# Kernel optimization log

Measured on AMD Instinct MI355X. Metric: run time of the kernel, lower is better.

The kernel has to match this reference:

```python
import jax, jax.numpy as jnp
import numpy as np

B, N, F_IN, F_OUT = 8, 2048, 256, 64
ALPHA = 0.2          # LeakyReLU negative slope
NEG_INF = -9e15      # matches -9000000000000000.0 in the torch code


def setup_inputs() -> dict:
    key = jax.random.key(0)
    k = jax.random.split(key, 7)
    x = jax.random.normal(k[0], (B, N, F_IN), dtype=jnp.float32)
    adj = jax.random.randint(k[1], (B, N, N), 0, 2, dtype=jnp.int32)
    # W: nn.Linear(in_features, out_features)
    W = jax.random.normal(k[2], (F_IN, F_OUT), dtype=jnp.float32) / np.sqrt(F_IN)
    b_W = jax.random.normal(k[3], (F_OUT,), dtype=jnp.float32) * 0.01
    # a: nn.Linear(2*out_features, 1); decomposed as a_src (first F_OUT rows,
    # multiplies h_i) and a_dst (last F_OUT rows, multiplies h_j) + bias.
    a_src = jax.random.normal(k[4], (F_OUT,), dtype=jnp.float32) / np.sqrt(2 * F_OUT)
    a_dst = jax.random.normal(k[5], (F_OUT,), dtype=jnp.float32) / np.sqrt(2 * F_OUT)
    a_b = jax.random.normal(k[6], (), dtype=jnp.float32) * 0.01
    return {"x": x, "adj": adj, "W": W, "b_W": b_W,
            "a_src": a_src, "a_dst": a_dst, "a_b": a_b}


def reference(x, adj, W, b_W, a_src, a_dst, a_b):
    # h = W(input): [B, N, F_OUT]
    h = jnp.einsum('bnf,fo->bno', x, W) + b_W
    # Additive attention decomposition: a([h_i || h_j]) = a_src.h_i + a_dst.h_j + b
    # (avoids materializing the [B, N, N, 2F] concat tensor of the original)
    src = jnp.einsum('bno,o->bn', h, a_src)  # row term  (h_i)
    dst = jnp.einsum('bno,o->bn', h, a_dst)  # col term  (h_j)
    e = jax.nn.leaky_relu(src[:, :, None] + dst[:, None, :] + a_b, ALPHA)  # [B,N,N]
    e = jnp.where(adj > 0, e, NEG_INF)
    attention = jax.nn.softmax(e, axis=2)
    h_prime = jnp.einsum('bij,bjo->bio', attention, h)  # [B, N, F_OUT]
    return jax.nn.elu(h_prime)  # concat=True branch
```

## Files before the change

### kernel.cpp

```cpp
#include <hip/hip_runtime.h>

#define B_   8
#define N_   2048
#define FIN  256
#define FOUT 64
#define ALPHA 0.2f

typedef __attribute__((ext_vector_type(8))) short bf16x8;
typedef __attribute__((ext_vector_type(8))) unsigned short u16x8;
typedef __attribute__((ext_vector_type(4))) unsigned short u16x4;
typedef __attribute__((ext_vector_type(4))) float f32x4;

__device__ __forceinline__ float b2f(unsigned short u) {
    union { unsigned int u; float f; } v; v.u = ((unsigned int)u) << 16; return v.f;
}
__device__ __forceinline__ unsigned short f2b(float f) {
    union { float f; unsigned int u; } v; v.f = f;
    unsigned int r = v.u + 0x7FFFu + ((v.u >> 16) & 1u);
    return (unsigned short)(r >> 16);
}

__global__ __launch_bounds__(256) void k_hgemm_tr(
    const float* __restrict__ x, const float* __restrict__ W,
    const float* __restrict__ bW, const float* __restrict__ asrc,
    const float* __restrict__ adst,
    unsigned short* __restrict__ hT, float* __restrict__ src, float* __restrict__ dst)
{
    __shared__ unsigned short tileT[FOUT * 20];
    __shared__ float as_s[FOUT], ad_s[FOUT];

    const int tid = threadIdx.x;
    const int wv = tid >> 6, lane = tid & 63;
    const int quad = lane >> 4, col = lane & 15;
    const int f = wv * 16 + col;

    if (tid < FOUT) { as_s[tid] = asrc[tid]; ad_s[tid] = adst[tid]; }

    bf16x8 Bf[8];
    #pragma unroll
    for (int kk = 0; kk < 8; ++kk) {
        bf16x8 t;
        #pragma unroll
        for (int j = 0; j < 8; ++j)
            t[j] = (short)f2b(W[(kk * 32 + quad * 8 + j) * FOUT + f]);
        Bf[kk] = t;
    }
    const float bias = bW[f];
    const int r0 = blockIdx.x * 16;
    const int b = r0 >> 11;
    const int j0b = r0 & (N_ - 1);

    f32x4 acc = {0.f, 0.f, 0.f, 0.f};
    #pragma unroll
    for (int kk = 0; kk < 8; ++kk) {
        const float* xp = x + (size_t)(r0 + col) * FIN + kk * 32 + quad * 8;
        float4 x0 = *(const float4*)xp;
        float4 x1 = *(const float4*)(xp + 4);
        bf16x8 Af;
        Af[0] = (short)f2b(x0.x); Af[1] = (short)f2b(x0.y);
        Af[2] = (short)f2b(x0.z); Af[3] = (short)f2b(x0.w);
        Af[4] = (short)f2b(x1.x); Af[5] = (short)f2b(x1.y);
        Af[6] = (short)f2b(x1.z); Af[7] = (short)f2b(x1.w);
        acc = __builtin_amdgcn_mfma_f32_16x16x32_bf16(Af, Bf[kk], acc, 0, 0, 0);
    }
    #pragma unroll
    for (int reg = 0; reg < 4; ++reg)
        tileT[f * 20 + quad * 4 + reg] = f2b(acc[reg] + bias);
    __syncthreads();

    {
        const int i = tid >> 4, fb = (tid & 15) * 4;
        float sp = 0.f, dp = 0.f;
        #pragma unroll
        for (int k = 0; k < 4; ++k) {
            float hv = b2f(tileT[(fb + k) * 20 + i]);
            sp += hv * as_s[fb + k]; dp += hv * ad_s[fb + k];
        }
        sp += __shfl_xor(sp, 1); sp += __shfl_xor(sp, 2);
        sp += __shfl_xor(sp, 4); sp += __shfl_xor(sp, 8);
        dp += __shfl_xor(dp, 1); dp += __shfl_xor(dp, 2);
        dp += __shfl_xor(dp, 4); dp += __shfl_xor(dp, 8);
        if ((tid & 15) == 0) { src[r0 + i] = sp; dst[r0 + i] = dp; }
    }
    {
        const int fq = tid >> 2, ic = (tid & 3) * 4;
        unsigned short* op = hT + (size_t)(b * FOUT + fq) * N_ + j0b + ic;
        *(u16x4*)op = *(const u16x4*)&tileT[fq * 20 + ic];
    }
}

#define ATT_TILE(Aa,Ab,Ac,Ad, An0,An1,An2,An3, BfC, BfN, BUF, JT)                      \
{                                                                                      \
                   \
    const float4 Dv0 = *(const float4*)(dstbase + (JT) * 128);                         \
    const float4 Dv1 = *(const float4*)(dstbase + (JT) * 128 + 4);                     \
    const float4 Dv2 = *(const float4*)(dstbase + (JT) * 128 + 8);                     \
    const float4 Dv3 = *(const float4*)(dstbase + (JT) * 128 + 12);                    \
    const int av[16] = {Aa.x,Aa.y,Aa.z,Aa.w, Ab.x,Ab.y,Ab.z,Ab.w,                      \
                        Ac.x,Ac.y,Ac.z,Ac.w, Ad.x,Ad.y,Ad.z,Ad.w};                     \
    const float dv[16] = {Dv0.x,Dv0.y,Dv0.z,Dv0.w, Dv1.x,Dv1.y,Dv1.z,Dv1.w,            \
                          Dv2.x,Dv2.y,Dv2.z,Dv2.w, Dv3.x,Dv3.y,Dv3.z,Dv3.w};           \
    u16x8 p0, p1; float ls = 0.f;                                                      \
    _Pragma("unroll")                                                                  \
    for (int k = 0; k < 16; ++k) {                                                     \
        float e = srci + dv[k];                                                        \
        e = e > 0.f ? e : ALPHA * e;                                                   \
        float wval = av[k] > 0 ? __expf(e) : 0.f;                                      \
        unsigned short wb = f2b(wval);                                                 \
        ls += b2f(wb);         \
        if (k < 8) p0[k] = wb; else p1[k - 8] = wb;                                    \
    }                                                                                  \
    lsum += ls;                                                                        \
    {   unsigned short* q = &w_s[BUF][il * 136 + jg * 16];                             \
        *(u16x8*)q = p0; *(u16x8*)(q + 8) = p1; }                                      \
    {                          \
        const int jn = (((JT) + 1) & 3) * 128;                                         \
        An0 = *(const int4*)(adjbase + jn);                                            \
        An1 = *(const int4*)(adjbase + jn + 4);                                        \
        An2 = *(const int4*)(adjbase + jn + 8);                                        \
        An3 = *(const int4*)(adjbase + jn + 12); }                                     \
                                   \
    asm volatile("s_waitcnt lgkmcnt(0)\n\ts_barrier" ::: "memory");                    \
    {                                        \
        const int jn = (((JT) + 1) & 3) * 128;                                         \
        BfN[0] = *(const bf16x8*)(hfbase + jn);                                        \
        BfN[1] = *(const bf16x8*)(hfbase + jn + 32);                                   \
        BfN[2] = *(const bf16x8*)(hfbase + jn + 64);                                   \
        BfN[3] = *(const bf16x8*)(hfbase + jn + 96); }                                 \
    _Pragma("unroll")                                                                  \
    for (int kk = 0; kk < 4; ++kk) {                                                   \
        bf16x8 A0 = *(const bf16x8*)&w_s[BUF][col * 136 + kk * 32 + quad * 8];         \
        bf16x8 A1 = *(const bf16x8*)&w_s[BUF][(16 + col) * 136 + kk * 32 + quad * 8];  \
        acc0 = __builtin_amdgcn_mfma_f32_16x16x32_bf16(A0, BfC[kk], acc0, 0, 0, 0);    \
        acc1 = __builtin_amdgcn_mfma_f32_16x16x32_bf16(A1, BfC[kk], acc1, 0, 0, 0);    \
    }                                                                                  \
}

__global__ __launch_bounds__(256, 4) void k_attn(
    const int* __restrict__ adj, const float* __restrict__ src,
    const float* __restrict__ dst, const unsigned short* __restrict__ hT,
    const float* __restrict__ abp,
    float* __restrict__ pnum, float* __restrict__ pden)
{
    __shared__ unsigned short w_s[2][32 * 136];
    __shared__ float src_s[32];

    const int tid = threadIdx.x;
    const int wv = tid >> 6, lane = tid & 63;
    const int quad = lane >> 4, col = lane & 15;
    const int s4 = blockIdx.x & 3;
    const int g  = blockIdx.x >> 2;
    const int b  = g >> 6;
    const int i0 = (g & 63) * 32;
    const int j0 = s4 * 512;

    if (tid < 32) src_s[tid] = src[b * N_ + i0 + tid];
    __syncthreads();

    const int il = tid >> 3, jg = tid & 7;
    const float srci = src_s[il] + abp[0];
    const int* adjbase = adj + (size_t)(b * N_ + i0 + il) * N_ + j0 + jg * 16;
    const float* dstbase = dst + b * N_ + j0 + jg * 16;
    const unsigned short* hfbase = hT + (size_t)(b * FOUT + wv * 16 + col) * N_ + j0 + quad * 8;

    int4 aE0 = *(const int4*)(adjbase);
    int4 aE1 = *(const int4*)(adjbase + 4);
    int4 aE2 = *(const int4*)(adjbase + 8);
    int4 aE3 = *(const int4*)(adjbase + 12);
    int4 aO0, aO1, aO2, aO3;
    bf16x8 bfE[4], bfO[4];
    bfE[0] = *(const bf16x8*)(hfbase);
    bfE[1] = *(const bf16x8*)(hfbase + 32);
    bfE[2] = *(const bf16x8*)(hfbase + 64);
    bfE[3] = *(const bf16x8*)(hfbase + 96);

    float lsum = 0.f;
    f32x4 acc0 = {0, 0, 0, 0}, acc1 = {0, 0, 0, 0};

    ATT_TILE(aE0, aE1, aE2, aE3, aO0, aO1, aO2, aO3, bfE, bfO, 0, 0)
    ATT_TILE(aO0, aO1, aO2, aO3, aE0, aE1, aE2, aE3, bfO, bfE, 1, 1)
    ATT_TILE(aE0, aE1, aE2, aE3, aO0, aO1, aO2, aO3, bfE, bfO, 0, 2)
    ATT_TILE(aO0, aO1, aO2, aO3, aE0, aE1, aE2, aE3, bfO, bfE, 1, 3)

    lsum += __shfl_xor(lsum, 1);
    lsum += __shfl_xor(lsum, 2);
    lsum += __shfl_xor(lsum, 4);
    if (jg == 0) pden[(size_t)blockIdx.x * 32 + il] = lsum;

    float* pb = pnum + (size_t)blockIdx.x * 2048 + wv * 16 + col;
    #pragma unroll
    for (int m = 0; m < 2; ++m) {
        f32x4 a = m ? acc1 : acc0;
        #pragma unroll
        for (int reg = 0; reg < 4; ++reg)
            pb[(m * 16 + quad * 4 + reg) * 64] = a[reg];
    }
}

__global__ __launch_bounds__(256) void k_reduce(
    const float* __restrict__ pnum, const float* __restrict__ pden,
    float* __restrict__ out)
{
    const int g = blockIdx.x;
    const int tid = threadIdx.x;
    const int f = tid & 63, ro = tid >> 6;
    const size_t base = (size_t)g * 4 * 2048;
    #pragma unroll
    for (int rr = 0; rr < 8; ++rr) {
        const int row = ro * 8 + rr;
        float num = 0.f, den = 0.f;
        #pragma unroll
        for (int s = 0; s < 4; ++s) {
            num += pnum[base + (size_t)s * 2048 + row * 64 + f];
            den += pden[(size_t)(g * 4 + s) * 32 + row];
        }
        den = den > 0.f ? den : 1.f;
        float v = num / den;
        v = v > 0.f ? v : (__expf(v) - 1.f);
        out[((size_t)g * 32 + row) * 64 + f] = v;
    }
}

extern "C" void kernel_launch(void* const* d_in, const int* in_sizes, int n_in,
                              void* d_out, int out_size, void* d_ws, size_t ws_size,
                              hipStream_t stream)
{
    const float* x    = (const float*)d_in[0];
    const int*   adj  = (const int*)d_in[1];
    const float* W    = (const float*)d_in[2];
    const float* bW   = (const float*)d_in[3];
    const float* asrc = (const float*)d_in[4];
    const float* adst = (const float*)d_in[5];
    const float* abp  = (const float*)d_in[6];
    float* out = (float*)d_out;

    char* ws = (char*)d_ws;
    unsigned short* hT = (unsigned short*)ws;
    float* src  = (float*)(ws + (size_t)2 * 1024 * 1024);
    float* dst  = (float*)(ws + (size_t)2 * 1024 * 1024 + 64 * 1024);
    float* pnum = (float*)(ws + (size_t)4 * 1024 * 1024);
    float* pden = (float*)(ws + (size_t)21 * 1024 * 1024);

    k_hgemm_tr<<<1024, 256, 0, stream>>>(x, W, bW, asrc, adst, hT, src, dst);
    k_attn<<<2048, 256, 0, stream>>>(adj, src, dst, hT, abp, pnum, pden);
    k_reduce<<<512, 256, 0, stream>>>(pnum, pden, out);
}
```

Before: 243.9 us.

## Compute attention weights directly in MFMA A-operand registers, removing LDS staging

The attention kernel now lays out adjacency loads so each lane computes exactly the bf16 weights it feeds as the MFMA A operand, which removes the shared-memory weight tile and the per-tile barriers. Each wave owns 16 rows and all 64 output features (four accumulators), with the block count halved and a register double-buffered loop over 32-column chunks. The reduce kernel is rewritten to use float4 loads over the new row-major partial layout. The cost is more hT loads per wave, since every wave reloads all 64 feature rows, plus higher register pressure and narrower 32-byte adjacency loads per lane.

```diff
diff --git a/kernel.cpp b/kernel.cpp
--- a/kernel.cpp
+++ b/kernel.cpp
@@ -5,6 +5,8 @@
 #define FIN  256
 #define FOUT 64
 #define ALPHA 0.2f
+#define NSP  4
+#define JC   (N_ / NSP / 32)
 
 typedef __attribute__((ext_vector_type(8))) short bf16x8;
 typedef __attribute__((ext_vector_type(8))) unsigned short u16x8;
@@ -89,111 +91,85 @@
     }
 }
 
-#define ATT_TILE(Aa,Ab,Ac,Ad, An0,An1,An2,An3, BfC, BfN, BUF, JT)                      \
-{                                                                                      \
-                   \
-    const float4 Dv0 = *(const float4*)(dstbase + (JT) * 128);                         \
-    const float4 Dv1 = *(const float4*)(dstbase + (JT) * 128 + 4);                     \
-    const float4 Dv2 = *(const float4*)(dstbase + (JT) * 128 + 8);                     \
-    const float4 Dv3 = *(const float4*)(dstbase + (JT) * 128 + 12);                    \
-    const int av[16] = {Aa.x,Aa.y,Aa.z,Aa.w, Ab.x,Ab.y,Ab.z,Ab.w,                      \
-                        Ac.x,Ac.y,Ac.z,Ac.w, Ad.x,Ad.y,Ad.z,Ad.w};                     \
-    const float dv[16] = {Dv0.x,Dv0.y,Dv0.z,Dv0.w, Dv1.x,Dv1.y,Dv1.z,Dv1.w,            \
-                          Dv2.x,Dv2.y,Dv2.z,Dv2.w, Dv3.x,Dv3.y,Dv3.z,Dv3.w};           \
-    u16x8 p0, p1; float ls = 0.f;                                                      \
-    _Pragma("unroll")                                                                  \
-    for (int k = 0; k < 16; ++k) {                                                     \
-        float e = srci + dv[k];                                                        \
-        e = e > 0.f ? e : ALPHA * e;                                                   \
-        float wval = av[k] > 0 ? __expf(e) : 0.f;                                      \
-        unsigned short wb = f2b(wval);                                                 \
-        ls += b2f(wb);         \
-        if (k < 8) p0[k] = wb; else p1[k - 8] = wb;                                    \
-    }                                                                                  \
-    lsum += ls;                                                                        \
-    {   unsigned short* q = &w_s[BUF][il * 136 + jg * 16];                             \
-        *(u16x8*)q = p0; *(u16x8*)(q + 8) = p1; }                                      \
-    {                          \
-        const int jn = (((JT) + 1) & 3) * 128;                                         \
-        An0 = *(const int4*)(adjbase + jn);                                            \
-        An1 = *(const int4*)(adjbase + jn + 4);                                        \
-        An2 = *(const int4*)(adjbase + jn + 8);                                        \
-        An3 = *(const int4*)(adjbase + jn + 12); }                                     \
-                                   \
-    asm volatile("s_waitcnt lgkmcnt(0)\n\ts_barrier" ::: "memory");                    \
-    {                                        \
-        const int jn = (((JT) + 1) & 3) * 128;                                         \
-        BfN[0] = *(const bf16x8*)(hfbase + jn);                                        \
-        BfN[1] = *(const bf16x8*)(hfbase + jn + 32);                                   \
-        BfN[2] = *(const bf16x8*)(hfbase + jn + 64);                                   \
-        BfN[3] = *(const bf16x8*)(hfbase + jn + 96); }                                 \
-    _Pragma("unroll")                                                                  \
-    for (int kk = 0; kk < 4; ++kk) {                                                   \
-        bf16x8 A0 = *(const bf16x8*)&w_s[BUF][col * 136 + kk * 32 + quad * 8];         \
-        bf16x8 A1 = *(const bf16x8*)&w_s[BUF][(16 + col) * 136 + kk * 32 + quad * 8];  \
-        acc0 = __builtin_amdgcn_mfma_f32_16x16x32_bf16(A0, BfC[kk], acc0, 0, 0, 0);    \
-        acc1 = __builtin_amdgcn_mfma_f32_16x16x32_bf16(A1, BfC[kk], acc1, 0, 0, 0);    \
-    }                                                                                  \
-}
-
-__global__ __launch_bounds__(256, 4) void k_attn(
+#define CHUNK(AEa, AEb, HE0, HE1, HE2, HE3, AOa, AOb, HO0, HO1, HO2, HO3, T)        \
+{                                                                                    \
+    const int jn = (((T) + 1) & (JC - 1)) * 32;                                      \
+    AOa = *(const int4*)(adjp + jn);                                                 \
+    AOb = *(const int4*)(adjp + jn + 4);                                             \
+    HO0 = *(const bf16x8*)(hfp + jn);                                                \
+    HO1 = *(const bf16x8*)(hfp + 16 * N_ + jn);                                      \
+    HO2 = *(const bf16x8*)(hfp + 32 * N_ + jn);                                      \
+    HO3 = *(const bf16x8*)(hfp + 48 * N_ + jn);                                      \
+    const int jc = (T) * 32;                                                         \
+    const float4 Dv0 = *(const float4*)(dstp + jc);                                  \
+    const float4 Dv1 = *(const float4*)(dstp + jc + 4);                              \
+    const int av[8] = {AEa.x, AEa.y, AEa.z, AEa.w, AEb.x, AEb.y, AEb.z, AEb.w};      \
+    const float dv[8] = {Dv0.x, Dv0.y, Dv0.z, Dv0.w, Dv1.x, Dv1.y, Dv1.z, Dv1.w};    \
+    bf16x8 Af; float ls = 0.f;                                                       \
+    _Pragma("unroll")                                                                \
+    for (int k = 0; k < 8; ++k) {                                                    \
+        float e = srci + dv[k];                                                      \
+        e = e > 0.f ? e : ALPHA * e;                                                 \
+        float wval = av[k] > 0 ? __expf(e) : 0.f;                                    \
+        unsigned short wb = f2b(wval);                                               \
+        ls += b2f(wb);       \
+        Af[k] = (short)wb;                                                           \
+    }                                                                                \
+    lsum += ls;                                                                      \
+    acc0 = __builtin_amdgcn_mfma_f32_16x16x32_bf16(Af, HE0, acc0, 0, 0, 0);          \
+    acc1 = __builtin_amdgcn_mfma_f32_16x16x32_bf16(Af, HE1, acc1, 0, 0, 0);          \
+    acc2 = __builtin_amdgcn_mfma_f32_16x16x32_bf16(Af, HE2, acc2, 0, 0, 0);          \
+    acc3 = __builtin_amdgcn_mfma_f32_16x16x32_bf16(Af, HE3, acc3, 0, 0, 0);          \
+}
+
+__global__ __launch_bounds__(256) void k_attn(
     const int* __restrict__ adj, const float* __restrict__ src,
     const float* __restrict__ dst, const unsigned short* __restrict__ hT,
     const float* __restrict__ abp,
     float* __restrict__ pnum, float* __restrict__ pden)
 {
-    __shared__ unsigned short w_s[2][32 * 136];
-    __shared__ float src_s[32];
-
     const int tid = threadIdx.x;
     const int wv = tid >> 6, lane = tid & 63;
     const int quad = lane >> 4, col = lane & 15;
-    const int s4 = blockIdx.x & 3;
-    const int g  = blockIdx.x >> 2;
-    const int b  = g >> 6;
-    const int i0 = (g & 63) * 32;
-    const int j0 = s4 * 512;
-
-    if (tid < 32) src_s[tid] = src[b * N_ + i0 + tid];
-    __syncthreads();
-
-    const int il = tid >> 3, jg = tid & 7;
-    const float srci = src_s[il] + abp[0];
-    const int* adjbase = adj + (size_t)(b * N_ + i0 + il) * N_ + j0 + jg * 16;
-    const float* dstbase = dst + b * N_ + j0 + jg * 16;
-    const unsigned short* hfbase = hT + (size_t)(b * FOUT + wv * 16 + col) * N_ + j0 + quad * 8;
-
-    int4 aE0 = *(const int4*)(adjbase);
-    int4 aE1 = *(const int4*)(adjbase + 4);
-    int4 aE2 = *(const int4*)(adjbase + 8);
-    int4 aE3 = *(const int4*)(adjbase + 12);
-    int4 aO0, aO1, aO2, aO3;
-    bf16x8 bfE[4], bfO[4];
-    bfE[0] = *(const bf16x8*)(hfbase);
-    bfE[1] = *(const bf16x8*)(hfbase + 32);
-    bfE[2] = *(const bf16x8*)(hfbase + 64);
-    bfE[3] = *(const bf16x8*)(hfbase + 96);
+    const int sp = blockIdx.x & 3;
+    const int rb = blockIdx.x >> 2;
+    const int grow0 = rb * 64 + wv * 16;
+    const int b = grow0 >> 11;
+    const int j0 = sp * 512;
+
+    const float srci = src[grow0 + col] + abp[0];
+    const int* adjp = adj + (size_t)(grow0 + col) * N_ + j0 + quad * 8;
+    const float* dstp = dst + (size_t)b * N_ + j0 + quad * 8;
+    const unsigned short* hfp = hT + ((size_t)b * FOUT + col) * N_ + j0 + quad * 8;
+
+    int4 aE0 = *(const int4*)(adjp);
+    int4 aE1 = *(const int4*)(adjp + 4);
+    bf16x8 hE0 = *(const bf16x8*)(hfp);
+    bf16x8 hE1 = *(const bf16x8*)(hfp + 16 * N_);
+    bf16x8 hE2 = *(const bf16x8*)(hfp + 32 * N_);
+    bf16x8 hE3 = *(const bf16x8*)(hfp + 48 * N_);
+    int4 aO0, aO1; bf16x8 hO0, hO1, hO2, hO3;
 
     float lsum = 0.f;
     f32x4 acc0 = {0, 0, 0, 0}, acc1 = {0, 0, 0, 0};
-
-    ATT_TILE(aE0, aE1, aE2, aE3, aO0, aO1, aO2, aO3, bfE, bfO, 0, 0)
-    ATT_TILE(aO0, aO1, aO2, aO3, aE0, aE1, aE2, aE3, bfO, bfE, 1, 1)
-    ATT_TILE(aE0, aE1, aE2, aE3, aO0, aO1, aO2, aO3, bfE, bfO, 0, 2)
-    ATT_TILE(aO0, aO1, aO2, aO3, aE0, aE1, aE2, aE3, bfO, bfE, 1, 3)
-
-    lsum += __shfl_xor(lsum, 1);
-    lsum += __shfl_xor(lsum, 2);
-    lsum += __shfl_xor(lsum, 4);
-    if (jg == 0) pden[(size_t)blockIdx.x * 32 + il] = lsum;
-
-    float* pb = pnum + (size_t)blockIdx.x * 2048 + wv * 16 + col;
-    #pragma unroll
-    for (int m = 0; m < 2; ++m) {
-        f32x4 a = m ? acc1 : acc0;
+    f32x4 acc2 = {0, 0, 0, 0}, acc3 = {0, 0, 0, 0};
+
+    for (int t = 0; t < JC; t += 2) {
+        CHUNK(aE0, aE1, hE0, hE1, hE2, hE3, aO0, aO1, hO0, hO1, hO2, hO3, t)
+        CHUNK(aO0, aO1, hO0, hO1, hO2, hO3, aE0, aE1, hE0, hE1, hE2, hE3, t + 1)
+    }
+
+    lsum += __shfl_xor(lsum, 16);
+    lsum += __shfl_xor(lsum, 32);
+    if (quad == 0) pden[(size_t)sp * (B_ * N_) + grow0 + col] = lsum;
+
+    float* pb = pnum + ((size_t)sp * (B_ * N_) + grow0) * FOUT;
+    #pragma unroll
+    for (int fg = 0; fg < 4; ++fg) {
+        f32x4 a = fg == 0 ? acc0 : fg == 1 ? acc1 : fg == 2 ? acc2 : acc3;
         #pragma unroll
         for (int reg = 0; reg < 4; ++reg)
-            pb[(m * 16 + quad * 4 + reg) * 64] = a[reg];
+            pb[(quad * 4 + reg) * FOUT + fg * 16 + col] = a[reg];
     }
 }
 
@@ -201,24 +177,23 @@
     const float* __restrict__ pnum, const float* __restrict__ pden,
     float* __restrict__ out)
 {
-    const int g = blockIdx.x;
-    const int tid = threadIdx.x;
-    const int f = tid & 63, ro = tid >> 6;
-    const size_t base = (size_t)g * 4 * 2048;
-    #pragma unroll
-    for (int rr = 0; rr < 8; ++rr) {
-        const int row = ro * 8 + rr;
-        float num = 0.f, den = 0.f;
-        #pragma unroll
-        for (int s = 0; s < 4; ++s) {
-            num += pnum[base + (size_t)s * 2048 + row * 64 + f];
-            den += pden[(size_t)(g * 4 + s) * 32 + row];
-        }
-        den = den > 0.f ? den : 1.f;
-        float v = num / den;
-        v = v > 0.f ? v : (__expf(v) - 1.f);
-        out[((size_t)g * 32 + row) * 64 + f] = v;
-    }
+    const int idx = blockIdx.x * 256 + threadIdx.x;
+    const int g = idx >> 4, f0 = (idx & 15) * 4;
+    float nx = 0.f, ny = 0.f, nz = 0.f, nw = 0.f, den = 0.f;
+    #pragma unroll
+    for (int s = 0; s < NSP; ++s) {
+        const float4 p = *(const float4*)&pnum[((size_t)s * (B_ * N_) + g) * FOUT + f0];
+        nx += p.x; ny += p.y; nz += p.z; nw += p.w;
+        den += pden[(size_t)s * (B_ * N_) + g];
+    }
+    den = den > 0.f ? den : 1.f;
+    float4 v;
+    v.x = nx / den; v.y = ny / den; v.z = nz / den; v.w = nw / den;
+    v.x = v.x > 0.f ? v.x : (__expf(v.x) - 1.f);
+    v.y = v.y > 0.f ? v.y : (__expf(v.y) - 1.f);
+    v.z = v.z > 0.f ? v.z : (__expf(v.z) - 1.f);
+    v.w = v.w > 0.f ? v.w : (__expf(v.w) - 1.f);
+    *(float4*)&out[(size_t)g * FOUT + f0] = v;
 }
 
 extern "C" void kernel_launch(void* const* d_in, const int* in_sizes, int n_in,
@@ -239,9 +214,9 @@
     float* src  = (float*)(ws + (size_t)2 * 1024 * 1024);
     float* dst  = (float*)(ws + (size_t)2 * 1024 * 1024 + 64 * 1024);
     float* pnum = (float*)(ws + (size_t)4 * 1024 * 1024);
-    float* pden = (float*)(ws + (size_t)21 * 1024 * 1024);
+    float* pden = (float*)(ws + (size_t)20 * 1024 * 1024);
 
     k_hgemm_tr<<<1024, 256, 0, stream>>>(x, W, bW, asrc, adst, hT, src, dst);
-    k_attn<<<2048, 256, 0, stream>>>(adj, src, dst, hT, abp, pnum, pden);
-    k_reduce<<<512, 256, 0, stream>>>(pnum, pden, out);
-}
+    k_attn<<<1024, 256, 0, stream>>>(adj, src, dst, hT, abp, pnum, pden);
+    k_reduce<<<1024, 256, 0, stream>>>(pnum, pden, out);
+}
```

Result: no change. 243.0 us (-0.4%).
